# Kernel tuning notes

Hardware: AMD Instinct MI355X
Metric: run time of the kernel (lower is better)

## Reference

```python
import jax, jax.numpy as jnp
import numpy as np

N_SIN = 3  # fcn_n_sin (static)


def setup_inputs() -> dict:
    key = jax.random.key(0)
    ks = jax.random.split(key, 5)
    B, I, O, H = 256, 128, 128, 32
    F = 1 + 2 * N_SIN
    return {
        "x": jax.random.normal(ks[0], (B, I), dtype=jnp.float32),
        "W1": jax.random.normal(ks[1], (I, O, H, F), dtype=jnp.float32) * 0.3,
        "W2": jax.random.normal(ks[2], (I, O, 1, H), dtype=jnp.float32) * 0.3,
        "B1": jax.random.normal(ks[3], (I, O, H), dtype=jnp.float32) * 0.1,
        "B2": jax.random.normal(ks[4], (I, O, 1), dtype=jnp.float32) * 0.1,
    }


def reference(x, W1, W2, B1, B2):
    # x: [B, I]; per-(i,o) edge MLP on a scalar input, summed over i.
    omega = (2.0 ** jnp.arange(N_SIN)).astype(x.dtype)          # [S]
    ox = x[..., None] * omega                                    # [B, I, S]
    feat = jnp.concatenate([x[..., None], jnp.sin(ox), jnp.cos(ox)], axis=-1)  # [B, I, 1+2S]
    # First linear: per-edge [F -> H]
    h = jnp.einsum('bif,iohf->bioh', feat, W1) + B1              # [B, I, O, H]
    h = jax.nn.silu(h)
    # Second linear: per-edge [H -> 1], then sum over input dims i
    out = jnp.einsum('bioh,ioh->bio', h, W2[:, :, 0, :]) + B2[:, :, 0]  # [B, I, O]
    return out.sum(axis=1)                                       # [B, O]
```

## Files before the change

kernel.cpp:

```cpp
#include <hip/hip_runtime.h>
#include <hip/hip_bf16.h>

#define B_DIM 256
#define I_DIM 128
#define O_DIM 128
#define H_DIM 32
#define F_DIM 7
#define ICHUNK 4
#define NCHUNK (I_DIM / ICHUNK)

typedef __attribute__((ext_vector_type(8))) short short8;
typedef __attribute__((ext_vector_type(4))) float float4v;

__device__ inline short bf16s(float v) {
    union { __hip_bfloat16 h; short s; } u;
    u.h = __float2bfloat16(v);
    return u.s;
}

template <int CTRL>
__device__ __forceinline__ float dppadd(float v) {
    int s = __builtin_amdgcn_update_dpp(0, __builtin_bit_cast(int, v),
                                        CTRL, 0xF, 0xF, true);
    return v + __builtin_bit_cast(float, s);
}
__device__ __forceinline__ float rowsum16(float v) {
    v = dppadd<0xB1>(v);
    v = dppadd<0x4E>(v);
    v = dppadd<0x141>(v);
    v = dppadd<0x140>(v);
    return v;
}

template <bool USE_WS>
__global__ __launch_bounds__(256, 4)
void fcnkan_mfma(const float* __restrict__ x,
                 const float* __restrict__ W1,
                 const float* __restrict__ W2,
                 const float* __restrict__ B1,
                 const float* __restrict__ B2,
                 float* __restrict__ ws,
                 float* __restrict__ out) {
    __shared__ __align__(16) short feat_s[ICHUNK * B_DIM * 8];
    __shared__ __align__(16) short w1_s[(ICHUNK * H_DIM + 1) * 8];
    __shared__ float b1_s[ICHUNK * H_DIM];
    __shared__ float w2_s[ICHUNK * H_DIM];

    const int tid  = threadIdx.x;
    const int o    = blockIdx.x;
    const int ic0  = blockIdx.y * ICHUNK;
    const int w    = tid >> 6;
    const int lane = tid & 63;
    const int m    = lane & 15;
    const int q    = lane >> 4;

    const short8 zero8 = {};
    const int ZROW = ICHUNK * H_DIM;

    {
        const float4* xp = reinterpret_cast<const float4*>(x + (size_t)tid * I_DIM + ic0);
        float4 x0 = xp[0];
        float xr[4] = {x0.x, x0.y, x0.z, x0.w};
        #pragma unroll
        for (int il = 0; il < ICHUNK; ++il) {
            float xv = xr[il];
            float s1 = __sinf(xv), c1 = __cosf(xv);
            float s2 = 2.f * s1 * c1, c2 = 1.f - 2.f * s1 * s1;
            float s4 = 2.f * s2 * c2, c4 = 1.f - 2.f * s2 * s2;
            short8 a;
            a[0] = bf16s(xv); a[1] = bf16s(s1); a[2] = bf16s(s2); a[3] = bf16s(s4);
            a[4] = bf16s(c1); a[5] = bf16s(c2); a[6] = bf16s(c4); a[7] = 0;
            *reinterpret_cast<short8*>(feat_s + (il * B_DIM + tid) * 8) = a;
        }
    }
    if (tid < ICHUNK * H_DIM) {
        int il = tid >> 5, h = tid & 31;
        size_t iobase = (size_t)(ic0 + il) * O_DIM + o;
        const float* wr = W1 + iobase * (H_DIM * F_DIM) + h * F_DIM;
        short8 bfr;
        #pragma unroll
        for (int f = 0; f < F_DIM; ++f) bfr[f] = bf16s(wr[f]);
        bfr[7] = 0;
        *reinterpret_cast<short8*>(w1_s + tid * 8) = bfr;
        b1_s[tid] = B1[iobase * H_DIM + h];
        w2_s[tid] = W2[iobase * H_DIM + h];
    }
    if (tid == 128) *reinterpret_cast<short8*>(w1_s + ZROW * 8) = zero8;
    __syncthreads();

    float acc[16];
    #pragma unroll
    for (int r = 0; r < 16; ++r) acc[r] = 0.f;

    #pragma unroll 1
    for (int il = 0; il < ICHUNK; ++il) {
        const short8* fS   = reinterpret_cast<const short8*>(feat_s) + il * B_DIM;
        const short8* wAll = reinterpret_cast<const short8*>(w1_s);

        short8 afrag[4];
        #pragma unroll
        for (int t = 0; t < 4; ++t)
            afrag[t] = fS[w * 64 + t * 16 + m];

        short8 bfrag[2];
        float  b1v[2], w2v[2];
        #pragma unroll
        for (int nt = 0; nt < 2; ++nt) {
            int h = nt * 16 + m;
            int idx = (q == 0) ? (il * H_DIM + h) : ZROW;
            bfrag[nt] = wAll[idx];
            b1v[nt] = b1_s[il * H_DIM + h];
            w2v[nt] = w2_s[il * H_DIM + h];
        }

        #pragma unroll
        for (int nt = 0; nt < 2; ++nt) {
            float4v c0 = {b1v[nt], b1v[nt], b1v[nt], b1v[nt]};
            #pragma unroll
            for (int t = 0; t < 4; ++t) {
                float4v z = __builtin_amdgcn_mfma_f32_16x16x32_bf16(
                    afrag[t], bfrag[nt], c0, 0, 0, 0);
                #pragma unroll
                for (int r = 0; r < 4; ++r) {
                    float zz = z[r];
                    float sg = __builtin_amdgcn_rcpf(1.f + __expf(-zz));
                    acc[t * 4 + r] = fmaf(zz * sg, w2v[nt], acc[t * 4 + r]);
                }
            }
        }
    }

    #pragma unroll
    for (int r = 0; r < 16; ++r) acc[r] = rowsum16(acc[r]);

    float b2c = 0.f;
    #pragma unroll
    for (int il = 0; il < ICHUNK; ++il) b2c += B2[(size_t)(ic0 + il) * O_DIM + o];

    if (m == 0) {
        if (USE_WS) {
            float* wsp = ws + ((size_t)blockIdx.y * O_DIM + o) * B_DIM;
            #pragma unroll
            for (int t = 0; t < 4; ++t)
                #pragma unroll
                for (int r = 0; r < 4; ++r)
                    wsp[w * 64 + t * 16 + q * 4 + r] = acc[t * 4 + r] + b2c;
        } else {
            #pragma unroll
            for (int t = 0; t < 4; ++t)
                #pragma unroll
                for (int r = 0; r < 4; ++r) {
                    int b = w * 64 + t * 16 + q * 4 + r;
                    atomicAdd(&out[(size_t)b * O_DIM + o], acc[t * 4 + r] + b2c);
                }
        }
    }
}

__global__ __launch_bounds__(256)
void reduce_kernel(const float* __restrict__ ws, float* __restrict__ out) {
    const int o = blockIdx.x;
    const int b = threadIdx.x;
    float s = 0.f;
    #pragma unroll
    for (int c = 0; c < NCHUNK; ++c)
        s += ws[((size_t)c * O_DIM + o) * B_DIM + b];
    out[(size_t)b * O_DIM + o] = s;
}

extern "C" void kernel_launch(void* const* d_in, const int* in_sizes, int n_in,
                              void* d_out, int out_size, void* d_ws, size_t ws_size,
                              hipStream_t stream) {
    const float* x  = (const float*)d_in[0];
    const float* W1 = (const float*)d_in[1];
    const float* W2 = (const float*)d_in[2];
    const float* B1 = (const float*)d_in[3];
    const float* B2 = (const float*)d_in[4];
    float* out = (float*)d_out;
    float* ws  = (float*)d_ws;

    const size_t ws_need = (size_t)NCHUNK * O_DIM * B_DIM * sizeof(float);
    dim3 grid(O_DIM, NCHUNK);
    if (ws_size >= ws_need) {
        fcnkan_mfma<true><<<grid, 256, 0, stream>>>(x, W1, W2, B1, B2, ws, out);
        reduce_kernel<<<O_DIM, B_DIM, 0, stream>>>(ws, out);
    } else {
        hipMemsetAsync(out, 0, (size_t)out_size * sizeof(float), stream);
        fcnkan_mfma<false><<<grid, 256, 0, stream>>>(x, W1, W2, B1, B2, ws, out);
    }
}
```

Before: 108.4 us.

## Process 16 inputs per block with double-buffered LDS prefetch of next sub-chunk

Each block now covers 16 input dims instead of 4, looping over four sub-chunks of 4. The next sub-chunk's x, W1, B1 and W2 loads are issued into registers before the current MFMA/SiLU work, then converted and written to the alternate LDS buffer. The aim is to hide global load latency and cut workspace size, write traffic and reduction work by a factor of four. In exchange the grid shrinks to 1024 blocks, which lowers parallelism, and the doubled LDS buffers plus extra live registers could hurt occupancy.

New measurement: 112.7 us. 4.0% more time.

```diff
diff --git a/kernel.cpp b/kernel.cpp
--- a/kernel.cpp
+++ b/kernel.cpp
@@ -6,8 +6,10 @@
 #define O_DIM 128
 #define H_DIM 32
 #define F_DIM 7
-#define ICHUNK 4
-#define NCHUNK (I_DIM / ICHUNK)
+#define IBLK 16
+#define SUB 4
+#define NSUB (IBLK / SUB)
+#define NCH_WS (I_DIM / IBLK)
 
 typedef __attribute__((ext_vector_type(8))) short short8;
 typedef __attribute__((ext_vector_type(4))) float float4v;
@@ -41,28 +43,44 @@
                  const float* __restrict__ B2,
                  float* __restrict__ ws,
                  float* __restrict__ out) {
-    __shared__ __align__(16) short feat_s[ICHUNK * B_DIM * 8];
-    __shared__ __align__(16) short w1_s[(ICHUNK * H_DIM + 1) * 8];
-    __shared__ float b1_s[ICHUNK * H_DIM];
-    __shared__ float w2_s[ICHUNK * H_DIM];
+    __shared__ __align__(16) short feat_s[2][SUB * B_DIM * 8];
+    __shared__ __align__(16) short w1_s[2][(SUB * H_DIM + 1) * 8];
+    __shared__ float b1_s[2][SUB * H_DIM];
+    __shared__ float w2_s[2][SUB * H_DIM];
 
     const int tid  = threadIdx.x;
     const int o    = blockIdx.x;
-    const int ic0  = blockIdx.y * ICHUNK;
+    const int i0   = blockIdx.y * IBLK;
     const int w    = tid >> 6;
     const int lane = tid & 63;
     const int m    = lane & 15;
     const int q    = lane >> 4;
 
     const short8 zero8 = {};
-    const int ZROW = ICHUNK * H_DIM;
-
+    const int ZROW = SUB * H_DIM;
+
+    if (tid == 254) {
+        *reinterpret_cast<short8*>(&w1_s[0][ZROW * 8]) = zero8;
+        *reinterpret_cast<short8*>(&w1_s[1][ZROW * 8]) = zero8;
+    }
+
+    const int pil = tid >> 5, ph = tid & 31;
+    const float4* xrow = reinterpret_cast<const float4*>(x + (size_t)tid * I_DIM + i0);
+
+    float4 px = xrow[0];
+    float wr[F_DIM], b1r = 0.f, w2r = 0.f;
+    if (tid < 128) {
+        size_t iob = ((size_t)(i0 + pil) * O_DIM + o);
+        const float* wp = W1 + iob * (H_DIM * F_DIM) + ph * F_DIM;
+        #pragma unroll
+        for (int f = 0; f < F_DIM; ++f) wr[f] = wp[f];
+        b1r = B1[iob * H_DIM + ph];
+        w2r = W2[iob * H_DIM + ph];
+    }
     {
-        const float4* xp = reinterpret_cast<const float4*>(x + (size_t)tid * I_DIM + ic0);
-        float4 x0 = xp[0];
-        float xr[4] = {x0.x, x0.y, x0.z, x0.w};
+        float xr[4] = {px.x, px.y, px.z, px.w};
         #pragma unroll
-        for (int il = 0; il < ICHUNK; ++il) {
+        for (int il = 0; il < SUB; ++il) {
             float xv = xr[il];
             float s1 = __sinf(xv), c1 = __cosf(xv);
             float s2 = 2.f * s1 * c1, c2 = 1.f - 2.f * s1 * s1;
@@ -70,22 +88,18 @@
             short8 a;
             a[0] = bf16s(xv); a[1] = bf16s(s1); a[2] = bf16s(s2); a[3] = bf16s(s4);
             a[4] = bf16s(c1); a[5] = bf16s(c2); a[6] = bf16s(c4); a[7] = 0;
-            *reinterpret_cast<short8*>(feat_s + (il * B_DIM + tid) * 8) = a;
-        }
-    }
-    if (tid < ICHUNK * H_DIM) {
-        int il = tid >> 5, h = tid & 31;
-        size_t iobase = (size_t)(ic0 + il) * O_DIM + o;
-        const float* wr = W1 + iobase * (H_DIM * F_DIM) + h * F_DIM;
-        short8 bfr;
-        #pragma unroll
-        for (int f = 0; f < F_DIM; ++f) bfr[f] = bf16s(wr[f]);
-        bfr[7] = 0;
-        *reinterpret_cast<short8*>(w1_s + tid * 8) = bfr;
-        b1_s[tid] = B1[iobase * H_DIM + h];
-        w2_s[tid] = W2[iobase * H_DIM + h];
-    }
-    if (tid == 128) *reinterpret_cast<short8*>(w1_s + ZROW * 8) = zero8;
+            *reinterpret_cast<short8*>(&feat_s[0][(il * B_DIM + tid) * 8]) = a;
+        }
+        if (tid < 128) {
+            short8 bfr;
+            #pragma unroll
+            for (int f = 0; f < F_DIM; ++f) bfr[f] = bf16s(wr[f]);
+            bfr[7] = 0;
+            *reinterpret_cast<short8*>(&w1_s[0][tid * 8]) = bfr;
+            b1_s[0][tid] = b1r;
+            w2_s[0][tid] = w2r;
+        }
+    }
     __syncthreads();
 
     float acc[16];
@@ -93,49 +107,92 @@
     for (int r = 0; r < 16; ++r) acc[r] = 0.f;
 
     #pragma unroll 1
-    for (int il = 0; il < ICHUNK; ++il) {
-        const short8* fS   = reinterpret_cast<const short8*>(feat_s) + il * B_DIM;
-        const short8* wAll = reinterpret_cast<const short8*>(w1_s);
-
-        short8 afrag[4];
-        #pragma unroll
-        for (int t = 0; t < 4; ++t)
-            afrag[t] = fS[w * 64 + t * 16 + m];
-
-        short8 bfrag[2];
-        float  b1v[2], w2v[2];
-        #pragma unroll
-        for (int nt = 0; nt < 2; ++nt) {
-            int h = nt * 16 + m;
-            int idx = (q == 0) ? (il * H_DIM + h) : ZROW;
-            bfrag[nt] = wAll[idx];
-            b1v[nt] = b1_s[il * H_DIM + h];
-            w2v[nt] = w2_s[il * H_DIM + h];
-        }
-
-        #pragma unroll
-        for (int nt = 0; nt < 2; ++nt) {
-            float4v c0 = {b1v[nt], b1v[nt], b1v[nt], b1v[nt]};
-            #pragma unroll
-            for (int t = 0; t < 4; ++t) {
-                float4v z = __builtin_amdgcn_mfma_f32_16x16x32_bf16(
-                    afrag[t], bfrag[nt], c0, 0, 0, 0);
-                #pragma unroll
-                for (int r = 0; r < 4; ++r) {
-                    float zz = z[r];
-                    float sg = __builtin_amdgcn_rcpf(1.f + __expf(-zz));
-                    acc[t * 4 + r] = fmaf(zz * sg, w2v[nt], acc[t * 4 + r]);
+    for (int s = 0; s < NSUB; ++s) {
+        const int p = s & 1;
+
+        if (s + 1 < NSUB) {
+            px = xrow[s + 1];
+            if (tid < 128) {
+                size_t iob = ((size_t)(i0 + (s + 1) * SUB + pil) * O_DIM + o);
+                const float* wp = W1 + iob * (H_DIM * F_DIM) + ph * F_DIM;
+                #pragma unroll
+                for (int f = 0; f < F_DIM; ++f) wr[f] = wp[f];
+                b1r = B1[iob * H_DIM + ph];
+                w2r = W2[iob * H_DIM + ph];
+            }
+        }
+
+        #pragma unroll 1
+        for (int il = 0; il < SUB; ++il) {
+            const short8* fS   = reinterpret_cast<const short8*>(&feat_s[p][0]) + il * B_DIM;
+            const short8* wAll = reinterpret_cast<const short8*>(&w1_s[p][0]);
+
+            short8 afrag[4];
+            #pragma unroll
+            for (int t = 0; t < 4; ++t)
+                afrag[t] = fS[w * 64 + t * 16 + m];
+
+            short8 bfrag[2];
+            float  b1v[2], w2v[2];
+            #pragma unroll
+            for (int nt = 0; nt < 2; ++nt) {
+                int h = nt * 16 + m;
+                int idx = (q == 0) ? (il * H_DIM + h) : ZROW;
+                bfrag[nt] = wAll[idx];
+                b1v[nt] = b1_s[p][il * H_DIM + h];
+                w2v[nt] = w2_s[p][il * H_DIM + h];
+            }
+
+            #pragma unroll
+            for (int nt = 0; nt < 2; ++nt) {
+                float4v c0 = {b1v[nt], b1v[nt], b1v[nt], b1v[nt]};
+                #pragma unroll
+                for (int t = 0; t < 4; ++t) {
+                    float4v z = __builtin_amdgcn_mfma_f32_16x16x32_bf16(
+                        afrag[t], bfrag[nt], c0, 0, 0, 0);
+                    #pragma unroll
+                    for (int r = 0; r < 4; ++r) {
+                        float zz = z[r];
+                        float sg = __builtin_amdgcn_rcpf(1.f + __expf(-zz));
+                        acc[t * 4 + r] = fmaf(zz * sg, w2v[nt], acc[t * 4 + r]);
+                    }
                 }
             }
         }
+
+        if (s + 1 < NSUB) {
+            const int pn = (s + 1) & 1;
+            float xr[4] = {px.x, px.y, px.z, px.w};
+            #pragma unroll
+            for (int il = 0; il < SUB; ++il) {
+                float xv = xr[il];
+                float s1 = __sinf(xv), c1 = __cosf(xv);
+                float s2 = 2.f * s1 * c1, c2 = 1.f - 2.f * s1 * s1;
+                float s4 = 2.f * s2 * c2, c4 = 1.f - 2.f * s2 * s2;
+                short8 a;
+                a[0] = bf16s(xv); a[1] = bf16s(s1); a[2] = bf16s(s2); a[3] = bf16s(s4);
+                a[4] = bf16s(c1); a[5] = bf16s(c2); a[6] = bf16s(c4); a[7] = 0;
+                *reinterpret_cast<short8*>(&feat_s[pn][(il * B_DIM + tid) * 8]) = a;
+            }
+            if (tid < 128) {
+                short8 bfr;
+                #pragma unroll
+                for (int f = 0; f < F_DIM; ++f) bfr[f] = bf16s(wr[f]);
+                bfr[7] = 0;
+                *reinterpret_cast<short8*>(&w1_s[pn][tid * 8]) = bfr;
+                b1_s[pn][tid] = b1r;
+                w2_s[pn][tid] = w2r;
+            }
+        }
+        __syncthreads();
     }
 
     #pragma unroll
     for (int r = 0; r < 16; ++r) acc[r] = rowsum16(acc[r]);
 
     float b2c = 0.f;
-    #pragma unroll
-    for (int il = 0; il < ICHUNK; ++il) b2c += B2[(size_t)(ic0 + il) * O_DIM + o];
+    #pragma unroll 1
+    for (int il = 0; il < IBLK; ++il) b2c += B2[(size_t)(i0 + il) * O_DIM + o];
 
     if (m == 0) {
         if (USE_WS) {
@@ -163,7 +220,7 @@
     const int b = threadIdx.x;
     float s = 0.f;
     #pragma unroll
-    for (int c = 0; c < NCHUNK; ++c)
+    for (int c = 0; c < NCH_WS; ++c)
         s += ws[((size_t)c * O_DIM + o) * B_DIM + b];
     out[(size_t)b * O_DIM + o] = s;
 }
@@ -179,8 +236,8 @@
     float* out = (float*)d_out;
     float* ws  = (float*)d_ws;
 
-    const size_t ws_need = (size_t)NCHUNK * O_DIM * B_DIM * sizeof(float);
-    dim3 grid(O_DIM, NCHUNK);
+    const size_t ws_need = (size_t)NCH_WS * O_DIM * B_DIM * sizeof(float);
+    dim3 grid(O_DIM, I_DIM / IBLK);
     if (ws_size >= ws_need) {
         fcnkan_mfma<true><<<grid, 256, 0, stream>>>(x, W1, W2, B1, B2, ws, out);
         reduce_kernel<<<O_DIM, B_DIM, 0, stream>>>(ws, out);
```
